# Performance work log

Measured on AMD Instinct MI355X. Metric: run time of the kernel, lower is better.

The kernel has to match this reference:

```python
import jax, jax.numpy as jnp
import numpy as np

B = 512          # batch
SIZE_IN = 1024   # input features
SIZE_OUT = 256   # output features
NUM_Q = 16       # quantiles


def setup_inputs() -> dict:
    key = jax.random.key(0)
    k1, k2, k3, k4 = jax.random.split(key, 4)
    x = jax.random.normal(k1, (B, SIZE_IN), dtype=jnp.float32)
    indices = jax.random.randint(k2, (B, SIZE_IN), 0, NUM_Q, dtype=jnp.int64)
    # param_index table: row (q*SIZE_IN + j) holds a SIZE_OUT weight vector
    param_table = jax.random.normal(k3, (NUM_Q * SIZE_IN, SIZE_OUT), dtype=jnp.float32)
    bias = jax.random.normal(k4, (SIZE_OUT,), dtype=jnp.float32)
    return {"x": x, "indices": indices, "param_table": param_table, "bias": bias}


def reference(x, indices, param_table, bias):
    size_in = x.shape[1]
    # flat row index into the quantile-indexed table: q*size_in + feature_pos
    flat_idx = indices * size_in + jnp.arange(size_in, dtype=indices.dtype)[None, :]  # [B, In]
    gathered = param_table[flat_idx]  # [B, In, Out] gather
    # scale each gathered weight vector by the scalar input and reduce over features
    out = jnp.einsum('bi,bio->bo', x, gathered)  # [B, Out]
    return out + bias
```

## Files before the change

kernel.cpp:

```cpp
#include <hip/hip_runtime.h>


constexpr int BATCH    = 512;
constexpr int SIZE_IN  = 1024;
constexpr int SIZE_OUT = 256;

constexpr int THREADS    = 256;
constexpr int WAVES      = THREADS / 64;
constexpr int I_PER_WAVE = SIZE_IN / WAVES;

__global__ __launch_bounds__(THREADS, 2)
void indexed_linear_kernel(const float* __restrict__ x,
                           const int*   __restrict__ idx,
                           const float* __restrict__ table,
                           const float* __restrict__ bias,
                           float*       __restrict__ out)
{
    __shared__ int2  xr[SIZE_IN];
    __shared__ float red[WAVES][SIZE_OUT];

    const int b    = blockIdx.x;
    const int tid  = threadIdx.x;
    const int wave = tid >> 6;
    const int lane = tid & 63;

    {
        const float4 xv = reinterpret_cast<const float4*>(x   + b * SIZE_IN)[tid];
        const int4   qv = reinterpret_cast<const int4*>(idx + b * SIZE_IN)[tid];
        const int ibase = tid * 4;
        xr[ibase + 0] = make_int2(__float_as_int(xv.x), (qv.x * SIZE_IN + ibase + 0) * SIZE_OUT);
        xr[ibase + 1] = make_int2(__float_as_int(xv.y), (qv.y * SIZE_IN + ibase + 1) * SIZE_OUT);
        xr[ibase + 2] = make_int2(__float_as_int(xv.z), (qv.z * SIZE_IN + ibase + 2) * SIZE_OUT);
        xr[ibase + 3] = make_int2(__float_as_int(xv.w), (qv.w * SIZE_IN + ibase + 3) * SIZE_OUT);
    }
    __syncthreads();

    float4 acc = make_float4(0.f, 0.f, 0.f, 0.f);
    const int j0    = wave * I_PER_WAVE;
    const int olane = lane * 4;

    #pragma unroll 8
    for (int j = 0; j < I_PER_WAVE; ++j) {
        const int2  p  = xr[j0 + j];
        const float xj = __int_as_float(p.x);
        const float4 w = *reinterpret_cast<const float4*>(table + p.y + olane);
        acc.x = fmaf(xj, w.x, acc.x);
        acc.y = fmaf(xj, w.y, acc.y);
        acc.z = fmaf(xj, w.z, acc.z);
        acc.w = fmaf(xj, w.w, acc.w);
    }

    *reinterpret_cast<float4*>(&red[wave][olane]) = acc;
    __syncthreads();

    float s = bias[tid];
    #pragma unroll
    for (int w = 0; w < WAVES; ++w) s += red[w][tid];
    out[b * SIZE_OUT + tid] = s;
}

extern "C" void kernel_launch(void* const* d_in, const int* in_sizes, int n_in,
                              void* d_out, int out_size, void* d_ws, size_t ws_size,
                              hipStream_t stream) {
    const float* x     = (const float*)d_in[0];
    const int*   idx   = (const int*)d_in[1];
    const float* table = (const float*)d_in[2];
    const float* bias  = (const float*)d_in[3];
    float*       out   = (float*)d_out;

    indexed_linear_kernel<<<dim3(BATCH), dim3(THREADS), 0, stream>>>(x, idx, table, bias, out);
}
```

Before: 90.32 us.

## Recast indexed gather as per-quantile masked bf16 MFMA GEMMs with atomic accumulation

Replaces the per-batch gather loop with a dense formulation. For each quantile q, the x rows are masked by (idx==q), packed to bf16 in LDS, and multiplied against that quantile's table slice with 16x16x32 bf16 MFMA instructions. Each block covers a 32-row batch tile, a 128-column output half and one quantile. Partial sums from the 16 quantiles are combined with atomicAdd into a zeroed output, and bias is added once. This removes the random row gathers in favour of streaming table reads and matrix-core compute, but does 16x more multiply work on mostly-zero inputs and rounds to bf16, which may affect accuracy.

```diff
diff --git a/kernel.cpp b/kernel.cpp
--- a/kernel.cpp
+++ b/kernel.cpp
@@ -1,62 +1,113 @@
 #include <hip/hip_runtime.h>
+#include <stdint.h>
 
 
-constexpr int BATCH    = 512;
 constexpr int SIZE_IN  = 1024;
 constexpr int SIZE_OUT = 256;
+constexpr int TM = 32;
+constexpr int TN = 128;
+constexpr int A_STRIDE = 1032;
 
-constexpr int THREADS    = 256;
-constexpr int WAVES      = THREADS / 64;
-constexpr int I_PER_WAVE = SIZE_IN / WAVES;
+typedef short short8   __attribute__((ext_vector_type(8)));
+typedef float floatx4  __attribute__((ext_vector_type(4)));
 
-__global__ __launch_bounds__(THREADS, 2)
-void indexed_linear_kernel(const float* __restrict__ x,
-                           const int*   __restrict__ idx,
-                           const float* __restrict__ table,
-                           const float* __restrict__ bias,
-                           float*       __restrict__ out)
+__device__ inline uint32_t pack2bf(float lo, float hi) {
+    uint32_t a = __float_as_uint(lo) + 0x8000u;
+    uint32_t b = __float_as_uint(hi) + 0x8000u;
+    return __builtin_amdgcn_perm(b, a, 0x07060302);
+}
+
+__global__ __launch_bounds__(256, 2)
+void idxlin_mfma(const float* __restrict__ x,
+                 const int*   __restrict__ idx,
+                 const float* __restrict__ table,
+                 const float* __restrict__ bias,
+                 float*       __restrict__ out)
 {
-    __shared__ int2  xr[SIZE_IN];
-    __shared__ float red[WAVES][SIZE_OUT];
+    __shared__ uint16_t Alds[TM * A_STRIDE];
 
-    const int b    = blockIdx.x;
-    const int tid  = threadIdx.x;
-    const int wave = tid >> 6;
-    const int lane = tid & 63;
+    const int tid = threadIdx.x;
+    const int q   = blockIdx.x & 15;
+    const int r   = blockIdx.x >> 4;
+    const int nh  = r & 1;
+    const int bt  = r >> 1;
+    const int b0  = bt * TM;
+    const int n0  = nh * TN;
 
-    {
-        const float4 xv = reinterpret_cast<const float4*>(x   + b * SIZE_IN)[tid];
-        const int4   qv = reinterpret_cast<const int4*>(idx + b * SIZE_IN)[tid];
-        const int ibase = tid * 4;
-        xr[ibase + 0] = make_int2(__float_as_int(xv.x), (qv.x * SIZE_IN + ibase + 0) * SIZE_OUT);
-        xr[ibase + 1] = make_int2(__float_as_int(xv.y), (qv.y * SIZE_IN + ibase + 1) * SIZE_OUT);
-        xr[ibase + 2] = make_int2(__float_as_int(xv.z), (qv.z * SIZE_IN + ibase + 2) * SIZE_OUT);
-        xr[ibase + 3] = make_int2(__float_as_int(xv.w), (qv.w * SIZE_IN + ibase + 3) * SIZE_OUT);
+    const float4* x4 = reinterpret_cast<const float4*>(x   + b0 * SIZE_IN);
+    const int4*   i4 = reinterpret_cast<const int4*>(idx + b0 * SIZE_IN);
+    #pragma unroll 4
+    for (int s = 0; s < TM; ++s) {
+        const int f = s * 256 + tid;
+        const float4 xv = x4[f];
+        const int4   iv = i4[f];
+        const float v0 = (iv.x == q) ? xv.x : 0.f;
+        const float v1 = (iv.y == q) ? xv.y : 0.f;
+        const float v2 = (iv.z == q) ? xv.z : 0.f;
+        const float v3 = (iv.w == q) ? xv.w : 0.f;
+        uint2 d;
+        d.x = pack2bf(v0, v1);
+        d.y = pack2bf(v2, v3);
+        *reinterpret_cast<uint2*>(&Alds[s * A_STRIDE + tid * 4]) = d;
     }
     __syncthreads();
 
-    float4 acc = make_float4(0.f, 0.f, 0.f, 0.f);
-    const int j0    = wave * I_PER_WAVE;
-    const int olane = lane * 4;
+    const int lane  = tid & 63;
+    const int w     = tid >> 6;
+    const int nlane = lane & 15;
+    const int quad  = lane >> 4;
 
-    #pragma unroll 8
-    for (int j = 0; j < I_PER_WAVE; ++j) {
-        const int2  p  = xr[j0 + j];
-        const float xj = __int_as_float(p.x);
-        const float4 w = *reinterpret_cast<const float4*>(table + p.y + olane);
-        acc.x = fmaf(xj, w.x, acc.x);
-        acc.y = fmaf(xj, w.y, acc.y);
-        acc.z = fmaf(xj, w.z, acc.z);
-        acc.w = fmaf(xj, w.w, acc.w);
+    const float* bp = table + (q * SIZE_IN + quad * 8) * SIZE_OUT + n0 + w * 32 + nlane;
+    const uint16_t* arow0 = &Alds[(0 * 16 + nlane) * A_STRIDE + quad * 8];
+    const uint16_t* arow1 = &Alds[(1 * 16 + nlane) * A_STRIDE + quad * 8];
+
+    floatx4 acc[2][2] = {{{0.f,0.f,0.f,0.f},{0.f,0.f,0.f,0.f}},
+                         {{0.f,0.f,0.f,0.f},{0.f,0.f,0.f,0.f}}};
+
+    #pragma unroll 2
+    for (int kb = 0; kb < SIZE_IN / 32; ++kb) {
+        float wv[2][8];
+        #pragma unroll
+        for (int nt = 0; nt < 2; ++nt)
+            #pragma unroll
+            for (int j = 0; j < 8; ++j)
+                wv[nt][j] = bp[j * SIZE_OUT + nt * 16];
+
+        const short8 a0 = *reinterpret_cast<const short8*>(arow0 + kb * 32);
+        const short8 a1 = *reinterpret_cast<const short8*>(arow1 + kb * 32);
+
+        #pragma unroll
+        for (int nt = 0; nt < 2; ++nt) {
+            union { uint32_t u[4]; short8 s; } bf;
+            bf.u[0] = pack2bf(wv[nt][0], wv[nt][1]);
+            bf.u[1] = pack2bf(wv[nt][2], wv[nt][3]);
+            bf.u[2] = pack2bf(wv[nt][4], wv[nt][5]);
+            bf.u[3] = pack2bf(wv[nt][6], wv[nt][7]);
+            acc[0][nt] = __builtin_amdgcn_mfma_f32_16x16x32_bf16(a0, bf.s, acc[0][nt], 0, 0, 0);
+            acc[1][nt] = __builtin_amdgcn_mfma_f32_16x16x32_bf16(a1, bf.s, acc[1][nt], 0, 0, 0);
+        }
+        bp += 32 * SIZE_OUT;
     }
 
-    *reinterpret_cast<float4*>(&red[wave][olane]) = acc;
-    __syncthreads();
+    #pragma unroll
+    for (int mt = 0; mt < 2; ++mt)
+        #pragma unroll
+        for (int nt = 0; nt < 2; ++nt)
+            #pragma unroll
+            for (int rr = 0; rr < 4; ++rr) {
+                const int bg = b0 + mt * 16 + quad * 4 + rr;
+                const int o  = n0 + w * 32 + nt * 16 + nlane;
+                atomicAdd(&out[bg * SIZE_OUT + o], acc[mt][nt][rr]);
+            }
 
-    float s = bias[tid];
-    #pragma unroll
-    for (int w = 0; w < WAVES; ++w) s += red[w][tid];
-    out[b * SIZE_OUT + tid] = s;
+    if (q == 0) {
+        const int o_l = tid & (TN - 1);
+        const int m0  = (tid >> 7) * 16;
+        const float bv = bias[n0 + o_l];
+        #pragma unroll
+        for (int rr = 0; rr < 16; ++rr)
+            atomicAdd(&out[(b0 + m0 + rr) * SIZE_OUT + n0 + o_l], bv);
+    }
 }
 
 extern "C" void kernel_launch(void* const* d_in, const int* in_sizes, int n_in,
@@ -68,5 +119,6 @@
     const float* bias  = (const float*)d_in[3];
     float*       out   = (float*)d_out;
 
-    indexed_linear_kernel<<<dim3(BATCH), dim3(THREADS), 0, stream>>>(x, idx, table, bias, out);
+    hipMemsetAsync(out, 0, (size_t)out_size * sizeof(float), stream);
+    idxlin_mfma<<<dim3(512), dim3(256), 0, stream>>>(x, idx, table, bias, out);
 }
```

Measured after the change: 91.41 us. About the same (+1.2%).
